# Performance work log

Measured on AMD Instinct MI355X. Metric: run time of the kernel, lower is better.

The kernel has to match this reference:

```python
import jax, jax.numpy as jnp
import numpy as np

B, N, K, H, C = 16, 2048, 9, 128, 2  # K = nb_neighbors, kernel_size = K+1


def setup_inputs() -> dict:
    key = jax.random.key(0)
    ks = jax.random.split(key, 7)
    s = 0.1
    x = jax.random.normal(ks[0], (B, N, C), jnp.float32)
    Wconv = jax.random.normal(ks[1], (H, C, K + 1), jnp.float32) * s  # conv1d weight
    bconv = jax.random.normal(ks[2], (H,), jnp.float32) * s
    W1 = jax.random.normal(ks[3], (H, C), jnp.float32) * s
    b1 = jax.random.normal(ks[4], (H,), jnp.float32) * s
    W2 = jax.random.normal(ks[5], (H, H), jnp.float32) * s
    b2 = jax.random.normal(ks[6], (H,), jnp.float32) * s
    return {"x": x, "Wconv": Wconv, "bconv": bconv, "W1": W1, "b1": b1, "W2": W2, "b2": b2}


def reference(x, Wconv, bconv, W1, b1, W2, b2):
    # node embedding: W1(x)
    node_emb = jnp.einsum('bnc,hc->bnh', x, W1) + b1  # (B,N,H)

    # pairwise Euclidean distances (B,N,N) via the GEMM form
    sq = jnp.sum(x * x, axis=-1)  # (B,N)
    d2 = sq[:, :, None] + sq[:, None, :] - 2.0 * jnp.einsum('bnc,bmc->bnm', x, x)
    dist = jnp.sqrt(jnp.maximum(d2, 0.0))

    # torch: topk(k=N) (descending) then take last K+1 columns -> the K+1
    # smallest distances ordered descending (nearest/self last)
    knn = jnp.flip(jnp.argsort(dist, axis=-1)[..., : K + 1], axis=-1)  # (B,N,K+1)

    # batched gather of neighbor coords: (B,N,K+1,C)
    coords = jax.vmap(lambda xb, ib: xb[ib])(x, knn)

    # conv1d with kernel spanning the full window -> single output position,
    # i.e. a contraction over (channel, position)
    conv_emb = jnp.einsum('bnkc,hck->bnh', coords, Wconv) + bconv  # (B,N,H)
    conv_emb = jnp.einsum('bnh,eh->bne', conv_emb, W2) + b2

    return node_emb + conv_emb
```

## Files before the change

### kernel.cpp

```cpp
#include <hip/hip_runtime.h>
#include <cfloat>
#include <stdint.h>

#define B_   16
#define N_   2048
#define KK   10
#define H_   128
#define SUB  32
#define NCH  (N_ / SUB)

#define RANK_BLOCKS (B_ * 32)
#define WEFF_OUT    (H_ * KK * 2 + H_)
#define WEFF_BLOCKS ((WEFF_OUT * 4) / 256)

__device__ inline uint32_t f32_ordered(float f) {
    uint32_t u = __float_as_uint(f);
    return (u & 0x80000000u) ? ~u : (u | 0x80000000u);
}

__global__ __launch_bounds__(256) void setup_kernel(
    const float* __restrict__ x,
    const float* __restrict__ Wconv, const float* __restrict__ bconv,
    const float* __restrict__ b1,    const float* __restrict__ W2,
    const float* __restrict__ b2,
    float4* __restrict__ xsorted,
    float*  __restrict__ weff,
    float*  __restrict__ btot)
{
#pragma clang fp contract(off)
    __shared__ __align__(16) uint64_t sk[N_];
    __shared__ int pcnt[4 * 64];
    const int tid = threadIdx.x;

    if (blockIdx.x >= RANK_BLOCKS) {
        const int g = (blockIdx.x - RANK_BLOCKS) * 256 + tid;
        const int o = g >> 2, q = g & 3;
        float acc = 0.f;
        if (o < H_ * KK * 2) {
            const int e = o / 20, r = o % 20, k = r >> 1, c = r & 1;
            const float* w2p = W2 + e * H_ + q * 32;
            const float* wcp = Wconv + (q * 32) * (2 * KK) + c * KK + k;
#pragma unroll 8
            for (int h = 0; h < 32; ++h)
                acc += w2p[h] * wcp[h * (2 * KK)];
        } else {
            const int e = o - H_ * KK * 2;
            const float* w2p = W2 + e * H_ + q * 32;
            const float* bcp = bconv + q * 32;
#pragma unroll 8
            for (int h = 0; h < 32; ++h) acc += w2p[h] * bcp[h];
        }
        acc += __shfl_xor(acc, 1, 64);
        acc += __shfl_xor(acc, 2, 64);
        if (q == 0) {
            if (o < H_ * KK * 2) weff[o] = acc;
            else {
                const int e = o - H_ * KK * 2;
                btot[e] = acc + b1[e] + b2[e];
            }
        }
        return;
    }

    const int b  = blockIdx.x >> 5;
    const int sg = blockIdx.x & 31;
    const float2* xb = (const float2*)(x + (size_t)b * N_ * 2);

    for (int i = tid; i < N_; i += 256)
        sk[i] = ((uint64_t)f32_ordered(xb[i].x) << 32) | (uint32_t)i;
    __syncthreads();

    const int el = tid & 63;
    const int pt = tid >> 6;
    const uint64_t kown = sk[sg * 64 + el];
    const ulonglong2* sk2 = (const ulonglong2*)sk + pt * 256;
    int cnt = 0;
#pragma unroll 2
    for (int j = 0; j < 256; j += 4) {
        ulonglong2 t0 = sk2[j + 0];
        ulonglong2 t1 = sk2[j + 1];
        ulonglong2 t2 = sk2[j + 2];
        ulonglong2 t3 = sk2[j + 3];
        cnt += (int)(t0.x < kown) + (int)(t0.y < kown)
             + (int)(t1.x < kown) + (int)(t1.y < kown)
             + (int)(t2.x < kown) + (int)(t2.y < kown)
             + (int)(t3.x < kown) + (int)(t3.y < kown);
    }
    pcnt[pt * 64 + el] = cnt;
    __syncthreads();

    if (tid < 64) {
        const int r = pcnt[tid] + pcnt[64 + tid] + pcnt[128 + tid] + pcnt[192 + tid];
        const int i = sg * 64 + tid;
        float2 p = xb[i];
        float sm = p.x * p.x + p.y * p.y;
        xsorted[(size_t)b * N_ + r] =
            make_float4(p.x, p.y, sm, __uint_as_float((uint32_t)i));
    }
}

__global__ __launch_bounds__(256, 2) void knn_conv_kernel(
    const float4* __restrict__ xsorted,
    const float* __restrict__ W1,
    const float* __restrict__ weff,
    const float* __restrict__ btot,
    float* __restrict__ out)
{
#pragma clang fp contract(off)
    __shared__ float4   xs4[N_];
    __shared__ uint64_t mkeys[32 * 81];
    __shared__ float    wcoord[32 * 21];
    __shared__ float    hbound[32 * 9];

    const int tid  = threadIdx.x;
    const int w    = tid >> 6;
    const int l    = tid & 63;
    const int q    = l & 31;
    const int hh   = l >> 5;
    const int b    = blockIdx.x >> 6;
    const int tile = blockIdx.x & 63;

    const float4* xb = xsorted + (size_t)b * N_;
    for (int i = tid; i < N_; i += 256) xs4[i] = xb[i];
    __syncthreads();

    const int    n  = tile * 32 + q;
    const float4 qv = xs4[n];
    const float  qx = qv.x, qy = qv.y, sqn = qv.z;
    const float  qa  = xs4[tile * 32].x;
    const float  qbx = xs4[tile * 32 + 31].x;

    const uint64_t KINIT = (((uint64_t)0x7F7FFFFFu) << 32) | 0x3FFFFFu;
    uint64_t hk[KK];
#pragma unroll
    for (int j = 0; j < KK; ++j) hk[j] = KINIT;
    float h9d  = FLT_MAX;
    float shb  = FLT_MAX;
    float gate = FLT_MAX;

    auto insert = [&](float dc, float cw, int m) {
        uint32_t oi = __float_as_uint(cw);
        uint64_t key = ((uint64_t)__float_as_uint(dc) << 32)
                     | (oi << 11) | (uint32_t)m;
        if (key < hk[KK - 1]) {
#pragma unroll
            for (int j = KK - 1; j >= 1; --j) {
                bool cj  = key < hk[j];
                bool cjm = key < hk[j - 1];
                hk[j] = cj ? (cjm ? hk[j - 1] : key) : hk[j];
            }
            hk[0] = (key < hk[0]) ? key : hk[0];
        }
        h9d  = __uint_as_float((uint32_t)(hk[KK - 1] >> 32));
        gate = fminf(h9d, shb);
    };

    auto scan_chunk = [&](int mc) {
        const int base = mc + hh;
#pragma unroll
        for (int jj = 0; jj < 4; ++jj) {
            const int m0 = base + jj * 8;
            float4 c0 = xs4[m0 + 0];
            float4 c1 = xs4[m0 + 2];
            float4 c2 = xs4[m0 + 4];
            float4 c3 = xs4[m0 + 6];
            float dc0, dc1, dc2, dc3;
            { float s = sqn + c0.z; float pr = qx * c0.x;
              float dt = __builtin_fmaf(qy, c0.y, pr);
              float d2 = __builtin_fmaf(-2.0f, dt, s); dc0 = d2 > 0.0f ? d2 : 0.0f; }
            { float s = sqn + c1.z; float pr = qx * c1.x;
              float dt = __builtin_fmaf(qy, c1.y, pr);
              float d2 = __builtin_fmaf(-2.0f, dt, s); dc1 = d2 > 0.0f ? d2 : 0.0f; }
            { float s = sqn + c2.z; float pr = qx * c2.x;
              float dt = __builtin_fmaf(qy, c2.y, pr);
              float d2 = __builtin_fmaf(-2.0f, dt, s); dc2 = d2 > 0.0f ? d2 : 0.0f; }
            { float s = sqn + c3.z; float pr = qx * c3.x;
              float dt = __builtin_fmaf(qy, c3.y, pr);
              float d2 = __builtin_fmaf(-2.0f, dt, s); dc3 = d2 > 0.0f ? d2 : 0.0f; }
            if (dc0 <= gate) insert(dc0, c0.w, m0 + 0);
            if (dc1 <= gate) insert(dc1, c1.w, m0 + 2);
            if (dc2 <= gate) insert(dc2, c2.w, m0 + 4);
            if (dc3 <= gate) insert(dc3, c3.w, m0 + 6);
        }
    };

    const int ct  = tile;
    const int a   = (w - ct) & 3;
    const int c1_ = ct + a;
    const int c2_ = c1_ - 4;
    int c_near = (a <= 2) ? c1_ : c2_;
    if (c1_ > NCH - 1) c_near = c2_;
    if (c2_ < 0)       c_near = c1_;
    scan_chunk(c_near * SUB);

    hbound[q * 9 + (w * 2 + hh)] = h9d;
    __syncthreads();
    {
        const float* hb = &hbound[q * 9];
        float m0 = fminf(hb[0], hb[1]);
        float m1 = fminf(hb[2], hb[3]);
        float m2 = fminf(hb[4], hb[5]);
        float m3 = fminf(hb[6], hb[7]);
        shb  = fminf(fminf(m0, m1), fminf(m2, m3));
        gate = fminf(h9d, shb);
    }

    int  cl = c_near - 4, cr = c_near + 4;
    bool la = (cl >= 0), ra = (cr <= NCH - 1);
    while (la || ra) {
        float wm = gate;
        wm = fmaxf(wm, __shfl_xor(wm, 1,  64));
        wm = fmaxf(wm, __shfl_xor(wm, 2,  64));
        wm = fmaxf(wm, __shfl_xor(wm, 4,  64));
        wm = fmaxf(wm, __shfl_xor(wm, 8,  64));
        wm = fmaxf(wm, __shfl_xor(wm, 16, 64));
        wm = fmaxf(wm, __shfl_xor(wm, 32, 64));
        float gl = la ? (qa - xs4[cl * SUB + SUB - 1].x) : FLT_MAX;
        float gr = ra ? (xs4[cr * SUB].x - qbx)          : FLT_MAX;
        bool pickL = la && (!ra || gl <= gr);
        if (pickL) {
            if (__builtin_fmaf(gl, gl, -4e-6f) > wm) la = false;
            else { scan_chunk(cl * SUB); cl -= 4; la = (cl >= 0); }
        } else {
            if (__builtin_fmaf(gr, gr, -4e-6f) > wm) ra = false;
            else { scan_chunk(cr * SUB); cr += 4; ra = (cr <= NCH - 1); }
        }
    }

    {
        const int mb = q * 81 + (w * 2 + hh) * 10;
#pragma unroll
        for (int j = 0; j < KK; ++j) mkeys[mb + j] = hk[j];
    }

    const int e = tid & 127;
    float we[20];
    {
        const float4* wp = (const float4*)(weff + e * 20);
#pragma unroll
        for (int r = 0; r < 5; ++r) {
            float4 v = wp[r];
            we[4 * r + 0] = v.x; we[4 * r + 1] = v.y;
            we[4 * r + 2] = v.z; we[4 * r + 3] = v.w;
        }
    }
    const float w1x = W1[e * 2 + 0];
    const float w1y = W1[e * 2 + 1];
    const float bt  = btot[e];
    __syncthreads();

    {
        const int qm = tid >> 3;
        const int r  = tid & 7;
        const int mb = qm * 81 + r * 10;
        int p = 0;
#pragma unroll
        for (int sel = 0; sel < KK; ++sel) {
            uint64_t v = (p < KK) ? mkeys[mb + p] : 0xFFFFFFFFFFFFFFFFull;
            uint64_t t1 = __shfl_xor((unsigned long long)v, 1, 64);
            uint64_t m1 = v  < t1 ? v  : t1;
            uint64_t t2 = __shfl_xor((unsigned long long)m1, 2, 64);
            uint64_t m2 = m1 < t2 ? m1 : t2;
            uint64_t t4 = __shfl_xor((unsigned long long)m2, 4, 64);
            uint64_t vm = m2 < t4 ? m2 : t4;
            if (v == vm) {
                ++p;
                float4 c = xs4[(int)(vm & 0x7FF)];
                const int k = (KK - 1) - sel;
                wcoord[qm * 21 + 2 * k + 0] = c.x;
                wcoord[qm * 21 + 2 * k + 1] = c.y;
            }
        }
    }
    __syncthreads();

    const int qb_ = tid >> 7;
    const size_t obase = (size_t)b * N_ * H_;
#pragma unroll
    for (int jj = 0; jj < 16; ++jj) {
        const int qq = qb_ + 2 * jj;
        float4 xq = xs4[tile * 32 + qq];
        uint32_t orig = __float_as_uint(xq.w);
        const float* wc = &wcoord[qq * 21];
        float acc = bt;
        acc += xq.x * w1x;
        acc += xq.y * w1y;
#pragma unroll
        for (int k = 0; k < KK; ++k) {
            acc += wc[2 * k + 0] * we[2 * k + 0];
            acc += wc[2 * k + 1] * we[2 * k + 1];
        }
        out[obase + (size_t)orig * H_ + e] = acc;
    }
}

extern "C" void kernel_launch(void* const* d_in, const int* in_sizes, int n_in,
                              void* d_out, int out_size, void* d_ws, size_t ws_size,
                              hipStream_t stream) {
    const float* x     = (const float*)d_in[0];
    const float* Wconv = (const float*)d_in[1];
    const float* bconv = (const float*)d_in[2];
    const float* W1    = (const float*)d_in[3];
    const float* b1    = (const float*)d_in[4];
    const float* W2    = (const float*)d_in[5];
    const float* b2    = (const float*)d_in[6];
    float* out  = (float*)d_out;
    float* weff = (float*)d_ws;
    float* btot = weff + H_ * KK * 2;
    float4* xsorted = (float4*)((char*)d_ws + 16384);

    setup_kernel<<<dim3(RANK_BLOCKS + WEFF_BLOCKS), dim3(256), 0, stream>>>(
        x, Wconv, bconv, b1, W2, b2, xsorted, weff, btot);
    knn_conv_kernel<<<dim3(B_ * NCH), dim3(256), 0, stream>>>(
        xsorted, W1, weff, btot, out);
}
```

Measured before the change: 169.0 us.

## Use persistent blocks with atomic work queue and 16-way neighbor search split

Replaces the one-block-per-tile launch with 512 persistent 512-thread blocks that pull tile work items from a global atomic counter. Items are ordered centre-out within each batch so the cost of the tiles is spread evenly. Each block reloads the batch's sorted points only when the batch changes. The per-query scan is now split across 16 half-wave groups instead of 8, using stride-8 chunks and a wider merge. This targets tail imbalance from uneven search cost and reduces repeated shared-memory loads, at the price of atomic traffic, extra barriers per item and more merge work.

```diff
diff --git a/kernel.cpp b/kernel.cpp
--- a/kernel.cpp
+++ b/kernel.cpp
@@ -12,6 +12,7 @@
 #define RANK_BLOCKS (B_ * 32)
 #define WEFF_OUT    (H_ * KK * 2 + H_)
 #define WEFF_BLOCKS ((WEFF_OUT * 4) / 256)
+#define NITEMS      (B_ * NCH)
 
 __device__ inline uint32_t f32_ordered(float f) {
     uint32_t u = __float_as_uint(f);
@@ -25,7 +26,8 @@
     const float* __restrict__ b2,
     float4* __restrict__ xsorted,
     float*  __restrict__ weff,
-    float*  __restrict__ btot)
+    float*  __restrict__ btot,
+    int*    __restrict__ gcnt)
 {
 #pragma clang fp contract(off)
     __shared__ __align__(16) uint64_t sk[N_];
@@ -33,6 +35,7 @@
     const int tid = threadIdx.x;
 
     if (blockIdx.x >= RANK_BLOCKS) {
+        if (blockIdx.x == RANK_BLOCKS && tid == 0) *gcnt = 0;
         const int g = (blockIdx.x - RANK_BLOCKS) * 256 + tid;
         const int o = g >> 2, q = g & 3;
         float acc = 0.f;
@@ -99,139 +102,26 @@
     }
 }
 
-__global__ __launch_bounds__(256, 2) void knn_conv_kernel(
+__global__ __launch_bounds__(512, 4) void knn_conv_kernel(
     const float4* __restrict__ xsorted,
     const float* __restrict__ W1,
     const float* __restrict__ weff,
     const float* __restrict__ btot,
+    int* __restrict__ gcnt,
     float* __restrict__ out)
 {
 #pragma clang fp contract(off)
     __shared__ float4   xs4[N_];
-    __shared__ uint64_t mkeys[32 * 81];
+    __shared__ uint64_t mkeys[32 * 161];
     __shared__ float    wcoord[32 * 21];
-    __shared__ float    hbound[32 * 9];
-
-    const int tid  = threadIdx.x;
-    const int w    = tid >> 6;
-    const int l    = tid & 63;
-    const int q    = l & 31;
-    const int hh   = l >> 5;
-    const int b    = blockIdx.x >> 6;
-    const int tile = blockIdx.x & 63;
-
-    const float4* xb = xsorted + (size_t)b * N_;
-    for (int i = tid; i < N_; i += 256) xs4[i] = xb[i];
-    __syncthreads();
-
-    const int    n  = tile * 32 + q;
-    const float4 qv = xs4[n];
-    const float  qx = qv.x, qy = qv.y, sqn = qv.z;
-    const float  qa  = xs4[tile * 32].x;
-    const float  qbx = xs4[tile * 32 + 31].x;
-
-    const uint64_t KINIT = (((uint64_t)0x7F7FFFFFu) << 32) | 0x3FFFFFu;
-    uint64_t hk[KK];
-#pragma unroll
-    for (int j = 0; j < KK; ++j) hk[j] = KINIT;
-    float h9d  = FLT_MAX;
-    float shb  = FLT_MAX;
-    float gate = FLT_MAX;
-
-    auto insert = [&](float dc, float cw, int m) {
-        uint32_t oi = __float_as_uint(cw);
-        uint64_t key = ((uint64_t)__float_as_uint(dc) << 32)
-                     | (oi << 11) | (uint32_t)m;
-        if (key < hk[KK - 1]) {
-#pragma unroll
-            for (int j = KK - 1; j >= 1; --j) {
-                bool cj  = key < hk[j];
-                bool cjm = key < hk[j - 1];
-                hk[j] = cj ? (cjm ? hk[j - 1] : key) : hk[j];
-            }
-            hk[0] = (key < hk[0]) ? key : hk[0];
-        }
-        h9d  = __uint_as_float((uint32_t)(hk[KK - 1] >> 32));
-        gate = fminf(h9d, shb);
-    };
-
-    auto scan_chunk = [&](int mc) {
-        const int base = mc + hh;
-#pragma unroll
-        for (int jj = 0; jj < 4; ++jj) {
-            const int m0 = base + jj * 8;
-            float4 c0 = xs4[m0 + 0];
-            float4 c1 = xs4[m0 + 2];
-            float4 c2 = xs4[m0 + 4];
-            float4 c3 = xs4[m0 + 6];
-            float dc0, dc1, dc2, dc3;
-            { float s = sqn + c0.z; float pr = qx * c0.x;
-              float dt = __builtin_fmaf(qy, c0.y, pr);
-              float d2 = __builtin_fmaf(-2.0f, dt, s); dc0 = d2 > 0.0f ? d2 : 0.0f; }
-            { float s = sqn + c1.z; float pr = qx * c1.x;
-              float dt = __builtin_fmaf(qy, c1.y, pr);
-              float d2 = __builtin_fmaf(-2.0f, dt, s); dc1 = d2 > 0.0f ? d2 : 0.0f; }
-            { float s = sqn + c2.z; float pr = qx * c2.x;
-              float dt = __builtin_fmaf(qy, c2.y, pr);
-              float d2 = __builtin_fmaf(-2.0f, dt, s); dc2 = d2 > 0.0f ? d2 : 0.0f; }
-            { float s = sqn + c3.z; float pr = qx * c3.x;
-              float dt = __builtin_fmaf(qy, c3.y, pr);
-              float d2 = __builtin_fmaf(-2.0f, dt, s); dc3 = d2 > 0.0f ? d2 : 0.0f; }
-            if (dc0 <= gate) insert(dc0, c0.w, m0 + 0);
-            if (dc1 <= gate) insert(dc1, c1.w, m0 + 2);
-            if (dc2 <= gate) insert(dc2, c2.w, m0 + 4);
-            if (dc3 <= gate) insert(dc3, c3.w, m0 + 6);
-        }
-    };
-
-    const int ct  = tile;
-    const int a   = (w - ct) & 3;
-    const int c1_ = ct + a;
-    const int c2_ = c1_ - 4;
-    int c_near = (a <= 2) ? c1_ : c2_;
-    if (c1_ > NCH - 1) c_near = c2_;
-    if (c2_ < 0)       c_near = c1_;
-    scan_chunk(c_near * SUB);
-
-    hbound[q * 9 + (w * 2 + hh)] = h9d;
-    __syncthreads();
-    {
-        const float* hb = &hbound[q * 9];
-        float m0 = fminf(hb[0], hb[1]);
-        float m1 = fminf(hb[2], hb[3]);
-        float m2 = fminf(hb[4], hb[5]);
-        float m3 = fminf(hb[6], hb[7]);
-        shb  = fminf(fminf(m0, m1), fminf(m2, m3));
-        gate = fminf(h9d, shb);
-    }
-
-    int  cl = c_near - 4, cr = c_near + 4;
-    bool la = (cl >= 0), ra = (cr <= NCH - 1);
-    while (la || ra) {
-        float wm = gate;
-        wm = fmaxf(wm, __shfl_xor(wm, 1,  64));
-        wm = fmaxf(wm, __shfl_xor(wm, 2,  64));
-        wm = fmaxf(wm, __shfl_xor(wm, 4,  64));
-        wm = fmaxf(wm, __shfl_xor(wm, 8,  64));
-        wm = fmaxf(wm, __shfl_xor(wm, 16, 64));
-        wm = fmaxf(wm, __shfl_xor(wm, 32, 64));
-        float gl = la ? (qa - xs4[cl * SUB + SUB - 1].x) : FLT_MAX;
-        float gr = ra ? (xs4[cr * SUB].x - qbx)          : FLT_MAX;
-        bool pickL = la && (!ra || gl <= gr);
-        if (pickL) {
-            if (__builtin_fmaf(gl, gl, -4e-6f) > wm) la = false;
-            else { scan_chunk(cl * SUB); cl -= 4; la = (cl >= 0); }
-        } else {
-            if (__builtin_fmaf(gr, gr, -4e-6f) > wm) ra = false;
-            else { scan_chunk(cr * SUB); cr += 4; ra = (cr <= NCH - 1); }
-        }
-    }
-
-    {
-        const int mb = q * 81 + (w * 2 + hh) * 10;
-#pragma unroll
-        for (int j = 0; j < KK; ++j) mkeys[mb + j] = hk[j];
-    }
+    __shared__ float    hbound[32 * 17];
+    __shared__ int      s_item;
+
+    const int tid = threadIdx.x;
+    const int w   = tid >> 6;
+    const int l   = tid & 63;
+    const int q   = l & 31;
+    const int hh  = l >> 5;
 
     const int e = tid & 127;
     float we[20];
@@ -247,50 +137,183 @@
     const float w1x = W1[e * 2 + 0];
     const float w1y = W1[e * 2 + 1];
     const float bt  = btot[e];
-    __syncthreads();
-
-    {
-        const int qm = tid >> 3;
-        const int r  = tid & 7;
-        const int mb = qm * 81 + r * 10;
-        int p = 0;
-#pragma unroll
-        for (int sel = 0; sel < KK; ++sel) {
-            uint64_t v = (p < KK) ? mkeys[mb + p] : 0xFFFFFFFFFFFFFFFFull;
-            uint64_t t1 = __shfl_xor((unsigned long long)v, 1, 64);
-            uint64_t m1 = v  < t1 ? v  : t1;
-            uint64_t t2 = __shfl_xor((unsigned long long)m1, 2, 64);
-            uint64_t m2 = m1 < t2 ? m1 : t2;
-            uint64_t t4 = __shfl_xor((unsigned long long)m2, 4, 64);
-            uint64_t vm = m2 < t4 ? m2 : t4;
-            if (v == vm) {
-                ++p;
-                float4 c = xs4[(int)(vm & 0x7FF)];
-                const int k = (KK - 1) - sel;
-                wcoord[qm * 21 + 2 * k + 0] = c.x;
-                wcoord[qm * 21 + 2 * k + 1] = c.y;
-            }
-        }
-    }
-    __syncthreads();
-
-    const int qb_ = tid >> 7;
-    const size_t obase = (size_t)b * N_ * H_;
-#pragma unroll
-    for (int jj = 0; jj < 16; ++jj) {
-        const int qq = qb_ + 2 * jj;
-        float4 xq = xs4[tile * 32 + qq];
-        uint32_t orig = __float_as_uint(xq.w);
-        const float* wc = &wcoord[qq * 21];
-        float acc = bt;
-        acc += xq.x * w1x;
-        acc += xq.y * w1y;
-#pragma unroll
-        for (int k = 0; k < KK; ++k) {
-            acc += wc[2 * k + 0] * we[2 * k + 0];
-            acc += wc[2 * k + 1] * we[2 * k + 1];
-        }
-        out[obase + (size_t)orig * H_ + e] = acc;
+
+    int cur_b = -1;
+    for (;;) {
+        __syncthreads();
+        if (tid == 0) s_item = atomicAdd(gcnt, 1);
+        __syncthreads();
+        const int item = s_item;
+        if (item >= NITEMS) break;
+        const int b = item >> 6;
+        const int u = item & 63;
+        const int ht = (u & 1) ? (32 - ((u + 1) >> 1)) : (32 + (u >> 1));
+
+        if (b != cur_b) {
+            const float4* xb = xsorted + (size_t)b * N_;
+            for (int i = tid; i < N_; i += 512) xs4[i] = xb[i];
+            cur_b = b;
+            __syncthreads();
+        }
+
+        const float4 qv = xs4[ht * 32 + q];
+        const float  qx = qv.x, qy = qv.y, sqn = qv.z;
+        const float  qa  = xs4[ht * 32].x;
+        const float  qbx = xs4[ht * 32 + 31].x;
+
+        const uint64_t KINIT = (((uint64_t)0x7F7FFFFFu) << 32) | 0x3FFFFFu;
+        uint64_t hk[KK];
+#pragma unroll
+        for (int j = 0; j < KK; ++j) hk[j] = KINIT;
+        float h9d  = FLT_MAX;
+        float shb  = FLT_MAX;
+        float gate = FLT_MAX;
+
+        auto insert = [&](float dc, float cw, int m) {
+            uint32_t oi = __float_as_uint(cw);
+            uint64_t key = ((uint64_t)__float_as_uint(dc) << 32)
+                         | (oi << 11) | (uint32_t)m;
+            if (key < hk[KK - 1]) {
+#pragma unroll
+                for (int j = KK - 1; j >= 1; --j) {
+                    bool cj  = key < hk[j];
+                    bool cjm = key < hk[j - 1];
+                    hk[j] = cj ? (cjm ? hk[j - 1] : key) : hk[j];
+                }
+                hk[0] = (key < hk[0]) ? key : hk[0];
+            }
+            h9d  = __uint_as_float((uint32_t)(hk[KK - 1] >> 32));
+            gate = fminf(h9d, shb);
+        };
+
+        auto scan_chunk = [&](int mc) {
+            const int base = mc + hh;
+#pragma unroll
+            for (int jj = 0; jj < 4; ++jj) {
+                const int m0 = base + jj * 8;
+                float4 c0 = xs4[m0 + 0];
+                float4 c1 = xs4[m0 + 2];
+                float4 c2 = xs4[m0 + 4];
+                float4 c3 = xs4[m0 + 6];
+                float dc0, dc1, dc2, dc3;
+                { float s = sqn + c0.z; float pr = qx * c0.x;
+                  float dt = __builtin_fmaf(qy, c0.y, pr);
+                  float d2 = __builtin_fmaf(-2.0f, dt, s); dc0 = d2 > 0.0f ? d2 : 0.0f; }
+                { float s = sqn + c1.z; float pr = qx * c1.x;
+                  float dt = __builtin_fmaf(qy, c1.y, pr);
+                  float d2 = __builtin_fmaf(-2.0f, dt, s); dc1 = d2 > 0.0f ? d2 : 0.0f; }
+                { float s = sqn + c2.z; float pr = qx * c2.x;
+                  float dt = __builtin_fmaf(qy, c2.y, pr);
+                  float d2 = __builtin_fmaf(-2.0f, dt, s); dc2 = d2 > 0.0f ? d2 : 0.0f; }
+                { float s = sqn + c3.z; float pr = qx * c3.x;
+                  float dt = __builtin_fmaf(qy, c3.y, pr);
+                  float d2 = __builtin_fmaf(-2.0f, dt, s); dc3 = d2 > 0.0f ? d2 : 0.0f; }
+                if (dc0 <= gate) insert(dc0, c0.w, m0 + 0);
+                if (dc1 <= gate) insert(dc1, c1.w, m0 + 2);
+                if (dc2 <= gate) insert(dc2, c2.w, m0 + 4);
+                if (dc3 <= gate) insert(dc3, c3.w, m0 + 6);
+            }
+        };
+
+        const int a8  = (w - ht) & 7;
+        const int c1_ = ht + a8;
+        const int c2_ = c1_ - 8;
+        int c_near = (a8 <= 4) ? c1_ : c2_;
+        if (c1_ > NCH - 1) c_near = c2_;
+        if (c2_ < 0)       c_near = c1_;
+        scan_chunk(c_near * SUB);
+
+        hbound[q * 17 + (w * 2 + hh)] = h9d;
+        __syncthreads();
+        {
+            const float* hb = &hbound[q * 17];
+            float m0 = fminf(hb[0],  hb[1]);
+            float m1 = fminf(hb[2],  hb[3]);
+            float m2 = fminf(hb[4],  hb[5]);
+            float m3 = fminf(hb[6],  hb[7]);
+            float m4 = fminf(hb[8],  hb[9]);
+            float m5 = fminf(hb[10], hb[11]);
+            float m6 = fminf(hb[12], hb[13]);
+            float m7 = fminf(hb[14], hb[15]);
+            shb = fminf(fminf(fminf(m0, m1), fminf(m2, m3)),
+                        fminf(fminf(m4, m5), fminf(m6, m7)));
+            gate = fminf(h9d, shb);
+        }
+
+        int  cl = c_near - 8, cr = c_near + 8;
+        bool la = (cl >= 0), ra = (cr <= NCH - 1);
+        while (la || ra) {
+            float wm = gate;
+            wm = fmaxf(wm, __shfl_xor(wm, 1,  64));
+            wm = fmaxf(wm, __shfl_xor(wm, 2,  64));
+            wm = fmaxf(wm, __shfl_xor(wm, 4,  64));
+            wm = fmaxf(wm, __shfl_xor(wm, 8,  64));
+            wm = fmaxf(wm, __shfl_xor(wm, 16, 64));
+            wm = fmaxf(wm, __shfl_xor(wm, 32, 64));
+            float gl = la ? (qa - xs4[cl * SUB + SUB - 1].x) : FLT_MAX;
+            float gr = ra ? (xs4[cr * SUB].x - qbx)          : FLT_MAX;
+            bool pickL = la && (!ra || gl <= gr);
+            if (pickL) {
+                if (__builtin_fmaf(gl, gl, -4e-6f) > wm) la = false;
+                else { scan_chunk(cl * SUB); cl -= 8; la = (cl >= 0); }
+            } else {
+                if (__builtin_fmaf(gr, gr, -4e-6f) > wm) ra = false;
+                else { scan_chunk(cr * SUB); cr += 8; ra = (cr <= NCH - 1); }
+            }
+        }
+
+        {
+            const int mb = q * 161 + (w * 2 + hh) * 10;
+#pragma unroll
+            for (int j = 0; j < KK; ++j) mkeys[mb + j] = hk[j];
+        }
+        __syncthreads();
+
+        {
+            const int qm = tid >> 4;
+            const int r  = tid & 15;
+            const int mb = qm * 161 + r * 10;
+            int p = 0;
+#pragma unroll
+            for (int sel = 0; sel < KK; ++sel) {
+                uint64_t v = (p < KK) ? mkeys[mb + p] : 0xFFFFFFFFFFFFFFFFull;
+                uint64_t t1 = __shfl_xor((unsigned long long)v, 1, 64);
+                uint64_t m1 = v  < t1 ? v  : t1;
+                uint64_t t2 = __shfl_xor((unsigned long long)m1, 2, 64);
+                uint64_t m2 = m1 < t2 ? m1 : t2;
+                uint64_t t4 = __shfl_xor((unsigned long long)m2, 4, 64);
+                uint64_t m4 = m2 < t4 ? m2 : t4;
+                uint64_t t8 = __shfl_xor((unsigned long long)m4, 8, 64);
+                uint64_t vm = m4 < t8 ? m4 : t8;
+                if (v == vm) {
+                    ++p;
+                    float4 c = xs4[(int)(vm & 0x7FF)];
+                    const int k = (KK - 1) - sel;
+                    wcoord[qm * 21 + 2 * k + 0] = c.x;
+                    wcoord[qm * 21 + 2 * k + 1] = c.y;
+                }
+            }
+        }
+        __syncthreads();
+
+        const int qb_ = tid >> 7;
+        const size_t obase = (size_t)b * N_ * H_;
+#pragma unroll
+        for (int jj = 0; jj < 8; ++jj) {
+            const int qq = qb_ + 4 * jj;
+            float4 xq = xs4[ht * 32 + qq];
+            uint32_t orig = __float_as_uint(xq.w);
+            const float* wc = &wcoord[qq * 21];
+            float acc = bt;
+            acc += xq.x * w1x;
+            acc += xq.y * w1y;
+#pragma unroll
+            for (int k = 0; k < KK; ++k) {
+                acc += wc[2 * k + 0] * we[2 * k + 0];
+                acc += wc[2 * k + 1] * we[2 * k + 1];
+            }
+            out[obase + (size_t)orig * H_ + e] = acc;
+        }
     }
 }
 
@@ -307,10 +330,11 @@
     float* out  = (float*)d_out;
     float* weff = (float*)d_ws;
     float* btot = weff + H_ * KK * 2;
+    int*   gcnt = (int*)((char*)d_ws + 12288);
     float4* xsorted = (float4*)((char*)d_ws + 16384);
 
     setup_kernel<<<dim3(RANK_BLOCKS + WEFF_BLOCKS), dim3(256), 0, stream>>>(
-        x, Wconv, bconv, b1, W2, b2, xsorted, weff, btot);
-    knn_conv_kernel<<<dim3(B_ * NCH), dim3(256), 0, stream>>>(
-        xsorted, W1, weff, btot, out);
+        x, Wconv, bconv, b1, W2, b2, xsorted, weff, btot, gcnt);
+    knn_conv_kernel<<<dim3(512), dim3(512), 0, stream>>>(
+        xsorted, W1, weff, btot, gcnt, out);
 }
```

After: 173.5 us. 1.03x slower.
